# Optimization experiments

Hardware: AMD Instinct MI355X
Metric: run time of the kernel (lower is better)

Reference implementation:

```python
import jax, jax.numpy as jnp
import numpy as np

B, T, D = 2, 2048, 2048
H, KV, DH = 16, 8, 128
N, W, K = 1024, 256, 8


def rotate_half(x):
    x1, x2 = x[..., : DH // 2], x[..., DH // 2 :]
    return jnp.concatenate((-x2, x1), axis=-1)


def setup_inputs() -> dict:
    key = jax.random.key(0)
    ks = jax.random.split(key, 10)
    hidden_states = jax.random.normal(ks[0], (B, T, D), dtype=jnp.float32)
    cos = jax.random.uniform(ks[1], (B, T, DH), dtype=jnp.float32, minval=-1.0, maxval=1.0)
    sin = jax.random.uniform(ks[2], (B, T, DH), dtype=jnp.float32, minval=-1.0, maxval=1.0)
    mem = jax.random.normal(ks[3], (B, N, D), dtype=jnp.float32)
    Wq = jax.random.normal(ks[4], (D, D), dtype=jnp.float32) * 0.02
    Wk = jax.random.normal(ks[5], (KV * DH, D), dtype=jnp.float32) * 0.02
    Wv = jax.random.normal(ks[6], (KV * DH, D), dtype=jnp.float32) * 0.02
    Wo = jax.random.normal(ks[7], (D, D), dtype=jnp.float32) * 0.02
    Wg = jnp.zeros((1, D), dtype=jnp.float32)          # module inits gate weight to zeros
    bg = jnp.full((1,), 2.0, dtype=jnp.float32)        # and gate bias to 2.0
    return dict(hidden_states=hidden_states, cos=cos, sin=sin, mem=mem,
                Wq=Wq, Wk=Wk, Wv=Wv, Wo=Wo, Wg=Wg, bg=bg)


def reference(hidden_states, cos, sin, mem, Wq, Wk, Wv, Wo, Wg, bg):
    scale = DH ** -0.5
    n_rep = H // KV
    # projections -> [B, heads, T, d_h]
    q = (hidden_states @ Wq.T).reshape(B, T, H, DH).transpose(0, 2, 1, 3)
    k = (hidden_states @ Wk.T).reshape(B, T, KV, DH).transpose(0, 2, 1, 3)
    v = (hidden_states @ Wv.T).reshape(B, T, KV, DH).transpose(0, 2, 1, 3)
    # rotary (cos/sin are [B,T,d_h] -> broadcast over heads)
    c, s = cos[:, None], sin[:, None]
    q = q * c + rotate_half(q) * s
    k = k * c + rotate_half(k) * s
    # GQA repeat kv heads
    k_local = jnp.repeat(k, n_rep, axis=1)
    v_local = jnp.repeat(v, n_rep, axis=1)
    # --- local sliding-window causal attention (dense TxT mask, as in SDPA path) ---
    row = jnp.arange(T)[:, None]
    col = jnp.arange(T)[None, :]
    allowed = (col <= row) & (col >= row - W + 1)
    bias = jnp.where(allowed, 0.0, -jnp.inf).astype(q.dtype)
    scores = jnp.einsum('bhtd,bhsd->bhts', q, k_local) * scale + bias
    o_local = jnp.einsum('bhts,bhsd->bhtd', jax.nn.softmax(scores, axis=-1), v_local)
    o_local = o_local.transpose(0, 2, 1, 3).reshape(B, T, D) @ Wo.T
    # --- memory retrieval path (memory is detached in the original) ---
    mem_c = jax.lax.stop_gradient(mem)
    k_mem = (mem_c @ Wk.T).reshape(B, N, KV, DH).transpose(0, 2, 1, 3)
    v_mem = (mem_c @ Wv.T).reshape(B, N, KV, DH).transpose(0, 2, 1, 3)
    k_mem = jnp.repeat(k_mem, n_rep, axis=1)  # [B,H,N,d_h]
    v_mem = jnp.repeat(v_mem, n_rep, axis=1)
    q_chunk = q.mean(axis=2)                  # [B,H,d_h]
    sim_chunk = jnp.einsum('bhd,bhnd->bhn', q_chunk, k_mem) * scale
    _, idx = jax.lax.top_k(sim_chunk, K)      # [B,H,K]
    k_sh = jnp.take_along_axis(k_mem, idx[..., None], axis=2)  # [B,H,K,d_h]
    v_sh = jnp.take_along_axis(v_mem, idx[..., None], axis=2)
    sim_tok = jnp.einsum('bhtd,bhkd->bhtk', q, k_sh) * scale
    o_mem = jnp.einsum('bhtk,bhkd->bhtd', jax.nn.softmax(sim_tok, axis=-1), v_sh)
    o_mem = o_mem.transpose(0, 2, 1, 3).reshape(B, T, D)
    # --- learned gate fusion ---
    g = jax.nn.sigmoid(hidden_states @ Wg.T + bg)  # [B,T,1]
    return g * o_local + (1.0 - g) * o_mem
```

## Files before the change

### kernel.cpp

```cpp
#include <hip/hip_runtime.h>
#include <stdint.h>

#define B_   2
#define T_   2048
#define D_   2048
#define H_   16
#define KV_  8
#define DH_  128
#define NMEM 1024
#define WWIN 256
#define KSEL 8
#define BT   (B_*T_)
#define KVSTR 2048
#define QKVSTR 4096

__constant__ const float kScale = 0.08838834764831845f;

typedef __attribute__((ext_vector_type(8))) short s16x8;
typedef __attribute__((ext_vector_type(4))) float f32x4;

__device__ inline unsigned short f2bf(float f) {
  union { float f; unsigned int u; } c; c.f = f;
  unsigned int u = c.u;
  unsigned int r = u + 0x7fffu + ((u >> 16) & 1u);
  return (unsigned short)(r >> 16);
}
__device__ inline float bf2f(unsigned short v) {
  union { unsigned int u; float f; } c; c.u = ((unsigned int)v) << 16;
  return c.f;
}
__device__ inline f32x4 fzero4() { f32x4 v; v[0]=0.f; v[1]=0.f; v[2]=0.f; v[3]=0.f; return v; }

__global__ __launch_bounds__(256) void conv_kernel(const float* __restrict__ src,
                                                   unsigned short* __restrict__ dst, int n) {
  int i = blockIdx.x * 256 + threadIdx.x;
  if (i * 4 >= n) return;
  float4 v = ((const float4*)src)[i];
  uint2 o;
  o.x = (unsigned)f2bf(v.x) | ((unsigned)f2bf(v.y) << 16);
  o.y = (unsigned)f2bf(v.z) | ((unsigned)f2bf(v.w) << 16);
  ((uint2*)dst)[i] = o;
}

#define AOFF(buf, half) ((buf)*32768 + (half)*16384)
#define BOFF(buf, half) (65536 + (buf)*32768 + (half)*16384)

#define PH_MFMA(P, BF) \
  { \
    _Pragma("unroll") \
    for (int mi = 0; mi < 2; ++mi) { \
      _Pragma("unroll") \
      for (int ni = 0; ni < 4; ++ni) { \
        acc[P][mi][ni] = __builtin_amdgcn_mfma_f32_16x16x32_bf16(af[mi][0], BF[ni][0], acc[P][mi][ni], 0, 0, 0); \
        acc[P][mi][ni] = __builtin_amdgcn_mfma_f32_16x16x32_bf16(af[mi][1], BF[ni][1], acc[P][mi][ni], 0, 0, 0); \
      } \
    } \
  }

template<int MODE>
__global__ __launch_bounds__(512, 2) void gemm256(const unsigned short* __restrict__ A,
                                                  const unsigned short* __restrict__ Bw,
                                                  int N, int K, int lda, int ldc,
                                                  unsigned short* __restrict__ Cb,
                                                  const float* __restrict__ g,
                                                  const unsigned short* __restrict__ omem,
                                                  float* __restrict__ dout) {
  __shared__ __align__(16) char lds[131072];
  const int tid = threadIdx.x;
  const int wv = tid >> 6, lane = tid & 63;
  const int l15 = lane & 15, lg = lane >> 4;
  const int wr = wv >> 1, wc = wv & 1;
  const int gx = gridDim.x;
  const int nwg = gx * gridDim.y;
  const int flat = blockIdx.y * gx + blockIdx.x;
  const int chunk = nwg >> 3;
  const int wg = (flat & 7) * chunk + (flat >> 3);
  const int bx = wg % gx, by = wg / gx;
  const int m0 = by * 256, n0 = bx * 256;
  const int NT = K >> 6;

  auto stage_half = [&](const unsigned short* base, int stride, int row0, int koff, int ldsoff) {
#pragma unroll
    for (int ld = 0; ld < 2; ++ld) {
      int s = ld * 512 + tid;
      int row = s >> 3, cs = s & 7;
      int cg = cs ^ (row & 7);
      const unsigned short* src = base + (size_t)(row0 + row) * stride + koff + cg * 8;
      __builtin_amdgcn_global_load_lds((const __attribute__((address_space(1))) void*)src,
          (__attribute__((address_space(3))) void*)(lds + ldsoff + ld * 8192 + wv * 1024), 16, 0, 0);
    }
  };
  auto rdA = [&](int buf, int half, int mi, int kk) -> s16x8 {
    int r = wr * 32 + mi * 16 + l15;
    int slot = (kk * 4 + lg) ^ (r & 7);
    return *(const s16x8*)(lds + AOFF(buf, half) + r * 128 + slot * 16);
  };
  auto rdB = [&](int buf, int half, int ni, int kk) -> s16x8 {
    int r = wc * 64 + ni * 16 + l15;
    int slot = (kk * 4 + lg) ^ (r & 7);
    return *(const s16x8*)(lds + BOFF(buf, half) + r * 128 + slot * 16);
  };

  f32x4 acc[4][2][4];
#pragma unroll
  for (int p = 0; p < 4; ++p)
#pragma unroll
    for (int mi = 0; mi < 2; ++mi)
#pragma unroll
      for (int ni = 0; ni < 4; ++ni) acc[p][mi][ni] = fzero4();

  stage_half(A,  lda, m0,       0,  AOFF(0, 0));
  stage_half(Bw, K,   n0,       0,  BOFF(0, 0));
  stage_half(A,  lda, m0 + 128, 0,  AOFF(0, 1));
  stage_half(Bw, K,   n0 + 128, 0,  BOFF(0, 1));
  stage_half(A,  lda, m0,       64, AOFF(1, 0));
  stage_half(Bw, K,   n0,       64, BOFF(1, 0));
  stage_half(A,  lda, m0 + 128, 64, AOFF(1, 1));
  asm volatile("s_waitcnt vmcnt(6)" ::: "memory");
  __builtin_amdgcn_s_barrier();

  int cur = 0;
  for (int t = 0; t < NT; ++t, cur ^= 1) {
    const int nxt = cur ^ 1;
    s16x8 af[2][2], b0f[4][2], b1f[4][2];
#pragma unroll
    for (int mi = 0; mi < 2; ++mi) {
      af[mi][0] = rdA(cur, 0, mi, 0);
      af[mi][1] = rdA(cur, 0, mi, 1);
    }
#pragma unroll
    for (int ni = 0; ni < 4; ++ni) {
      b0f[ni][0] = rdB(cur, 0, ni, 0);
      b0f[ni][1] = rdB(cur, 0, ni, 1);
    }
    if (t + 1 < NT) stage_half(Bw, K, n0 + 128, (t + 1) * 64, BOFF(nxt, 1));
    __builtin_amdgcn_sched_barrier(0);
    __builtin_amdgcn_s_barrier();
    asm volatile("s_waitcnt lgkmcnt(0)" ::: "memory");
    __builtin_amdgcn_sched_barrier(0);
    __builtin_amdgcn_s_setprio(1);
    PH_MFMA(0, b0f);
    __builtin_amdgcn_s_setprio(0);
    __builtin_amdgcn_s_barrier();
#pragma unroll
    for (int ni = 0; ni < 4; ++ni) {
      b1f[ni][0] = rdB(cur, 1, ni, 0);
      b1f[ni][1] = rdB(cur, 1, ni, 1);
    }
    if (t + 2 < NT) stage_half(A, lda, m0, (t + 2) * 64, AOFF(cur, 0));
    __builtin_amdgcn_sched_barrier(0);
    __builtin_amdgcn_s_barrier();
    asm volatile("s_waitcnt lgkmcnt(0)" ::: "memory");
    __builtin_amdgcn_sched_barrier(0);
    __builtin_amdgcn_s_setprio(1);
    PH_MFMA(1, b1f);
    __builtin_amdgcn_s_setprio(0);
    __builtin_amdgcn_s_barrier();
#pragma unroll
    for (int mi = 0; mi < 2; ++mi) {
      af[mi][0] = rdA(cur, 1, mi, 0);
      af[mi][1] = rdA(cur, 1, mi, 1);
    }
    if (t + 2 < NT) stage_half(Bw, K, n0, (t + 2) * 64, BOFF(cur, 0));
    __builtin_amdgcn_sched_barrier(0);
    __builtin_amdgcn_s_barrier();
    asm volatile("s_waitcnt lgkmcnt(0)" ::: "memory");
    __builtin_amdgcn_sched_barrier(0);
    __builtin_amdgcn_s_setprio(1);
    PH_MFMA(2, b0f);
    __builtin_amdgcn_s_setprio(0);
    __builtin_amdgcn_s_barrier();
    if (t + 2 < NT) stage_half(A, lda, m0 + 128, (t + 2) * 64, AOFF(cur, 1));
    __builtin_amdgcn_sched_barrier(0);
    __builtin_amdgcn_s_barrier();
    __builtin_amdgcn_s_setprio(1);
    PH_MFMA(3, b1f);
    __builtin_amdgcn_s_setprio(0);
    if (t < NT - 2) asm volatile("s_waitcnt vmcnt(6)" ::: "memory");
    else            asm volatile("s_waitcnt vmcnt(0)" ::: "memory");
    __builtin_amdgcn_s_barrier();
  }

#pragma unroll
  for (int p = 0; p < 4; ++p)
#pragma unroll
    for (int mi = 0; mi < 2; ++mi)
#pragma unroll
      for (int ni = 0; ni < 4; ++ni)
#pragma unroll
        for (int j = 0; j < 4; ++j) {
          int row_g = m0 + (p >> 1) * 128 + wr * 32 + mi * 16 + lg * 4 + j;
          int col_g = n0 + (p & 1) * 128 + wc * 64 + ni * 16 + l15;
          float v = acc[p][mi][ni][j];
          size_t o = (size_t)row_g * ldc + col_g;
          if constexpr (MODE == 0) {
            Cb[o] = f2bf(v);
          } else {
            float gv = g[row_g];
            dout[o] = gv * v + (1.f - gv) * bf2f(omem[o]);
          }
        }
}

template<int MODE>
__global__ __launch_bounds__(256) void gemm_bt(const unsigned short* __restrict__ A,
                                               const unsigned short* __restrict__ Bw,
                                               int N, int K, int lda, int ldc,
                                               unsigned short* __restrict__ Cb,
                                               const float* __restrict__ g,
                                               const unsigned short* __restrict__ omem,
                                               float* __restrict__ dout) {
  __shared__ __align__(16) unsigned short sA[128 * 32];
  __shared__ __align__(16) unsigned short sB[128 * 32];
  const int tid = threadIdx.x;
  const int wv = tid >> 6, lane = tid & 63;
  const int gx = gridDim.x;
  const int nwg = gx * gridDim.y;
  const int flat = blockIdx.y * gx + blockIdx.x;
  const int chunk = nwg >> 3;
  const int wg = (flat & 7) * chunk + (flat >> 3);
  const int bx = wg % gx, by = wg / gx;
  const int m0 = by * 128, n0 = bx * 128;
  const int wr = wv >> 1, wc = wv & 1;
  const int l15 = lane & 15, lg = lane >> 4;
  const int rowA = tid >> 2;
  const int colB = (tid & 3) * 16;
  f32x4 acc[4][4];
#pragma unroll
  for (int mi = 0; mi < 4; ++mi)
#pragma unroll
    for (int ni = 0; ni < 4; ++ni) acc[mi][ni] = fzero4();

  char* sAc = (char*)sA;
  char* sBc = (char*)sB;
  for (int k0 = 0; k0 < K; k0 += 32) {
#pragma unroll
    for (int e = 0; e < 2; ++e) {
      const char* ga = (const char*)(A + ((size_t)(m0 + rowA + e * 64) * lda + k0)) + colB;
      __builtin_amdgcn_global_load_lds((const __attribute__((address_space(1))) void*)ga,
          (__attribute__((address_space(3))) void*)(sAc + e * 4096 + wv * 1024), 16, 0, 0);
      const char* gb = (const char*)(Bw + ((size_t)(n0 + rowA + e * 64) * K + k0)) + colB;
      __builtin_amdgcn_global_load_lds((const __attribute__((address_space(1))) void*)gb,
          (__attribute__((address_space(3))) void*)(sBc + e * 4096 + wv * 1024), 16, 0, 0);
    }
    __syncthreads();
    s16x8 af[4], bf_[4];
#pragma unroll
    for (int mi = 0; mi < 4; ++mi)
      af[mi] = *(const s16x8*)&sA[(wr * 64 + mi * 16 + l15) * 32 + lg * 8];
#pragma unroll
    for (int ni = 0; ni < 4; ++ni)
      bf_[ni] = *(const s16x8*)&sB[(wc * 64 + ni * 16 + l15) * 32 + lg * 8];
#pragma unroll
    for (int mi = 0; mi < 4; ++mi)
#pragma unroll
      for (int ni = 0; ni < 4; ++ni)
        acc[mi][ni] = __builtin_amdgcn_mfma_f32_16x16x32_bf16(af[mi], bf_[ni], acc[mi][ni], 0, 0, 0);
    __syncthreads();
  }
#pragma unroll
  for (int mi = 0; mi < 4; ++mi)
#pragma unroll
    for (int ni = 0; ni < 4; ++ni)
#pragma unroll
      for (int j = 0; j < 4; ++j) {
        int row_g = m0 + wr * 64 + mi * 16 + lg * 4 + j;
        int col_g = n0 + wc * 64 + ni * 16 + l15;
        float v = acc[mi][ni][j];
        size_t o = (size_t)row_g * ldc + col_g;
        if constexpr (MODE == 0) {
          Cb[o] = f2bf(v);
        } else {
          float gv = g[row_g];
          float om = bf2f(omem[o]);
          dout[o] = gv * v + (1.f - gv) * om;
        }
      }
}

__global__ __launch_bounds__(256) void rope_ip_kernel(unsigned short* __restrict__ buf,
                                                      const float* __restrict__ cosp,
                                                      const float* __restrict__ sinp,
                                                      int logp, int stride, int nthreads) {
  int i = blockIdx.x * 256 + threadIdx.x;
  if (i >= nthreads) return;
  int pp = i * 8;
  int row = pp >> logp;
  int p0 = pp & ((1 << logp) - 1);
  int blk = p0 >> 6, dd0 = p0 & 63;
  int b = row >> 11, t = row & 2047;
  const float* cb = cosp + ((size_t)b * T_ + t) * DH_;
  const float* sb = sinp + ((size_t)b * T_ + t) * DH_;
  unsigned short* p1 = buf + (size_t)row * stride + blk * 128 + dd0;
  s16x8 a = *(s16x8*)p1;
  s16x8 b8 = *(s16x8*)(p1 + 64);
  s16x8 o1, o2;
#pragma unroll
  for (int e = 0; e < 8; ++e) {
    float c1 = cb[dd0 + e], s1 = sb[dd0 + e];
    float c2 = cb[dd0 + 64 + e], s2 = sb[dd0 + 64 + e];
    float x1 = bf2f((unsigned short)a[e]), x2 = bf2f((unsigned short)b8[e]);
    o1[e] = (short)f2bf(x1 * c1 - x2 * s1);
    o2[e] = (short)f2bf(x2 * c2 + x1 * s2);
  }
  *(s16x8*)p1 = o1;
  *(s16x8*)(p1 + 64) = o2;
}

__global__ __launch_bounds__(256) void cs_kernel(const float* __restrict__ hs,
                                                 const float* __restrict__ cosp,
                                                 const float* __restrict__ sinp,
                                                 float* __restrict__ Cp, float* __restrict__ Sp) {
  __shared__ __align__(16) float hsL[32][128];
  __shared__ __align__(16) float csL[32][32];
  __shared__ __align__(16) float snL[32][32];
  const int tid = threadIdx.x;
  const int j0 = blockIdx.x * 128, d0 = blockIdx.y * 32;
  const int b = blockIdx.z >> 3, sp = blockIdx.z & 7;
  const int dq = (tid & 7) * 4;
  const int jq = (tid >> 3) * 4;
  float4 aC[4], aS[4];
#pragma unroll
  for (int a = 0; a < 4; ++a) {
    aC[a] = make_float4(0.f, 0.f, 0.f, 0.f);
    aS[a] = make_float4(0.f, 0.f, 0.f, 0.f);
  }
  const int csrow = tid >> 3, csc4 = tid & 7;
  for (int tile = 0; tile < 8; ++tile) {
    int t0 = sp * 256 + tile * 32;
    const float4* hs4 = (const float4*)(hs + ((size_t)b * T_ + t0) * D_ + j0);
#pragma unroll
    for (int r = 0; r < 4; ++r) {
      int i = tid + r * 256;
      int row = i >> 5, c4 = i & 31;
      *(float4*)&hsL[row][c4 * 4] = hs4[(size_t)row * (D_ / 4) + c4];
    }
    const float4* cp4 = (const float4*)(cosp + ((size_t)b * T_ + t0) * DH_ + d0);
    const float4* sp4 = (const float4*)(sinp + ((size_t)b * T_ + t0) * DH_ + d0);
    *(float4*)&csL[csrow][csc4 * 4] = cp4[(size_t)csrow * (DH_ / 4) + csc4];
    *(float4*)&snL[csrow][csc4 * 4] = sp4[(size_t)csrow * (DH_ / 4) + csc4];
    __syncthreads();
#pragma unroll 8
    for (int tt = 0; tt < 32; ++tt) {
      float4 cv = *(const float4*)&csL[tt][dq];
      float4 sv = *(const float4*)&snL[tt][dq];
      float4 hv = *(const float4*)&hsL[tt][jq];
      float ca[4] = {cv.x, cv.y, cv.z, cv.w};
      float sa[4] = {sv.x, sv.y, sv.z, sv.w};
#pragma unroll
      for (int a = 0; a < 4; ++a) {
        aC[a].x += ca[a] * hv.x; aC[a].y += ca[a] * hv.y;
        aC[a].z += ca[a] * hv.z; aC[a].w += ca[a] * hv.w;
        aS[a].x += sa[a] * hv.x; aS[a].y += sa[a] * hv.y;
        aS[a].z += sa[a] * hv.z; aS[a].w += sa[a] * hv.w;
      }
    }
    __syncthreads();
  }
#pragma unroll
  for (int a = 0; a < 4; ++a) {
    size_t o = ((size_t)(sp * B_ + b) * DH_ + d0 + dq + a) * D_ + j0 + jq;
    *(float4*)&Cp[o] = aC[a];
    *(float4*)&Sp[o] = aS[a];
  }
}

__global__ __launch_bounds__(256) void reduce_cs_kernel(const float4* __restrict__ Cp,
                                                        const float4* __restrict__ Sp,
                                                        float4* __restrict__ Cr,
                                                        float4* __restrict__ Sr) {
  int i = blockIdx.x * 256 + threadIdx.x;
  const int str = (B_ * DH_ * D_) / 4;
  float4 c = Cp[i], s = Sp[i];
#pragma unroll
  for (int p = 1; p < 8; ++p) {
    float4 cp = Cp[i + (size_t)p * str], sq = Sp[i + (size_t)p * str];
    c.x += cp.x; c.y += cp.y; c.z += cp.z; c.w += cp.w;
    s.x += sq.x; s.y += sq.y; s.z += sq.z; s.w += sq.w;
  }
  Cr[i] = c; Sr[i] = s;
}

__global__ __launch_bounds__(256) void qchunk_kernel(const float* __restrict__ Wq,
                                                     const float* __restrict__ Cr,
                                                     const float* __restrict__ Sr,
                                                     float* __restrict__ qc) {
  int gid = blockIdx.x * 256 + threadIdx.x;
  int wid = gid >> 6, lane = gid & 63;
  int b = wid >> 11, rem = wid & 2047;
  int h = rem >> 7, d = rem & 127;
  const float* w1 = Wq + (size_t)(h * DH_ + d) * D_;
  int dp = (d < 64) ? d + 64 : d - 64;
  float sgn = (d < 64) ? -1.f : 1.f;
  const float* w2 = Wq + (size_t)(h * DH_ + dp) * D_;
  const float* crow = Cr + ((size_t)b * DH_ + d) * D_;
  const float* srow = Sr + ((size_t)b * DH_ + d) * D_;
  float a1 = 0.f, a2 = 0.f;
  for (int j = lane; j < D_; j += 64) { a1 += w1[j] * crow[j]; a2 += w2[j] * srow[j]; }
#pragma unroll
  for (int off = 1; off < 64; off <<= 1) { a1 += __shfl_xor(a1, off); a2 += __shfl_xor(a2, off); }
  if (lane == 0) qc[wid] = (a1 + sgn * a2) * (1.f / (float)T_);
}

__global__ __launch_bounds__(256) void zk_kernel(const float* __restrict__ qc,
                                                 const float* __restrict__ Wk,
                                                 float* __restrict__ z) {
  int j = blockIdx.x * 256 + threadIdx.x;
  int h = blockIdx.y, b = blockIdx.z;
  int kvh = h >> 1;
  const float* qcl = qc + ((size_t)b * H_ + h) * DH_;
  const float* wb = Wk + (size_t)kvh * DH_ * D_ + j;
  float acc = 0.f;
#pragma unroll 8
  for (int d = 0; d < 128; ++d) acc += qcl[d] * wb[(size_t)d * D_];
  z[((size_t)b * H_ + h) * D_ + j] = acc;
}

__global__ __launch_bounds__(256) void sim_kernel(const float* __restrict__ z,
                                                  const float* __restrict__ mem,
                                                  float* __restrict__ sim) {
  __shared__ float4 mL[16 * 512];
  int tid = threadIdx.x;
  int n0 = blockIdx.x * 16, b = blockIdx.y;
  const float4* mem4 = (const float4*)(mem + (size_t)b * NMEM * D_);
#pragma unroll
  for (int c = 0; c < 32; ++c) {
    int i = tid + c * 256;
    int r = i >> 9, j4 = i & 511;
    mL[r * 512 + (j4 ^ (r & 7))] = mem4[(size_t)(n0 + r) * 512 + j4];
  }
  __syncthreads();
  int h = tid >> 4, n = tid & 15;
  const float4* zr = (const float4*)(z + ((size_t)b * H_ + h) * D_);
  float acc = 0.f;
  for (int j4 = 0; j4 < 512; ++j4) {
    float4 zz = zr[j4];
    float4 mm = mL[n * 512 + (j4 ^ (n & 7))];
    acc += zz.x * mm.x + zz.y * mm.y + zz.z * mm.z + zz.w * mm.w;
  }
  sim[((size_t)b * H_ + h) * NMEM + n0 + n] = acc * kScale;
}

__global__ __launch_bounds__(256) void topk_kernel(const float* __restrict__ sim,
                                                   int* __restrict__ idx) {
  __shared__ float sL[1024];
  __shared__ float rv[256];
  __shared__ int ri[256];
  int tid = threadIdx.x;
  int h = blockIdx.x, b = blockIdx.y;
  const float* sp = sim + ((size_t)b * H_ + h) * NMEM;
#pragma unroll
  for (int r = 0; r < 4; ++r) sL[tid + r * 256] = sp[tid + r * 256];
  __syncthreads();
  for (int kk = 0; kk < 8; ++kk) {
    float bv = -INFINITY; int bi = 0x7fffffff;
#pragma unroll
    for (int r = 0; r < 4; ++r) {
      int i = tid + r * 256;
      float v = sL[i];
      if (v > bv || (v == bv && i < bi)) { bv = v; bi = i; }
    }
    rv[tid] = bv; ri[tid] = bi;
    __syncthreads();
    for (int s = 128; s > 0; s >>= 1) {
      if (tid < s) {
        float v2 = rv[tid + s]; int i2 = ri[tid + s];
        if (v2 > rv[tid] || (v2 == rv[tid] && i2 < ri[tid])) { rv[tid] = v2; ri[tid] = i2; }
      }
      __syncthreads();
    }
    if (tid == 0) { idx[((size_t)b * H_ + h) * KSEL + kk] = ri[0]; sL[ri[0]] = -INFINITY; }
    __syncthreads();
  }
}

__global__ __launch_bounds__(256) void memattn_kernel(const unsigned short* __restrict__ qbf,
                                                      const unsigned short* __restrict__ kvmem,
                                                      const int* __restrict__ idx,
                                                      unsigned short* __restrict__ omem) {
  __shared__ float kl[8][128];
  __shared__ float vl[8][128];
  __shared__ int selL[8];
  int tid = threadIdx.x;
  int b = blockIdx.z, h = blockIdx.y, t = blockIdx.x * 256 + tid;
  int kvh = h >> 1;
  if (tid < 8) selL[tid] = idx[((size_t)b * H_ + h) * KSEL + tid];
  __syncthreads();
  {
    int r = tid >> 5, c4 = (tid & 31) * 4;
    size_t rb = ((size_t)b * NMEM + selL[r]) * (size_t)KVSTR;
    ushort4 k4 = *(const ushort4*)(kvmem + rb + kvh * DH_ + c4);
    ushort4 v4 = *(const ushort4*)(kvmem + rb + KV_ * DH_ + kvh * DH_ + c4);
    kl[r][c4 + 0] = bf2f(k4.x); kl[r][c4 + 1] = bf2f(k4.y);
    kl[r][c4 + 2] = bf2f(k4.z); kl[r][c4 + 3] = bf2f(k4.w);
    vl[r][c4 + 0] = bf2f(v4.x); vl[r][c4 + 1] = bf2f(v4.y);
    vl[r][c4 + 2] = bf2f(v4.z); vl[r][c4 + 3] = bf2f(v4.w);
  }
  __syncthreads();
  float sc[8] = {0.f,0.f,0.f,0.f,0.f,0.f,0.f,0.f};
  const unsigned short* qr = qbf + (size_t)(b * T_ + t) * QKVSTR + h * DH_;
  for (int c = 0; c < 4; ++c) {
    const s16x8* qp = (const s16x8*)(qr + c * 32);
#pragma unroll
    for (int u = 0; u < 4; ++u) {
      s16x8 q8 = qp[u];
#pragma unroll
      for (int e = 0; e < 8; ++e) {
        float qv = bf2f((unsigned short)q8[e]);
        int d = c * 32 + u * 8 + e;
#pragma unroll
        for (int kk = 0; kk < 8; ++kk) sc[kk] += qv * kl[kk][d];
      }
    }
  }
  float sm[8], mx = -INFINITY;
#pragma unroll
  for (int kk = 0; kk < 8; ++kk) { sm[kk] = sc[kk] * kScale; mx = fmaxf(mx, sm[kk]); }
  float sum = 0.f;
#pragma unroll
  for (int kk = 0; kk < 8; ++kk) { sm[kk] = __expf(sm[kk] - mx); sum += sm[kk]; }
  float inv = 1.f / sum;
#pragma unroll
  for (int kk = 0; kk < 8; ++kk) sm[kk] *= inv;
  unsigned short* orow = omem + (size_t)(b * T_ + t) * D_ + h * DH_;
  for (int d = 0; d < 128; d += 4) {
    float o0 = 0.f, o1 = 0.f, o2 = 0.f, o3 = 0.f;
#pragma unroll
    for (int kk = 0; kk < 8; ++kk) {
      float w = sm[kk];
      o0 += w * vl[kk][d + 0];
      o1 += w * vl[kk][d + 1];
      o2 += w * vl[kk][d + 2];
      o3 += w * vl[kk][d + 3];
    }
    uint2 pk;
    pk.x = (unsigned)f2bf(o0) | ((unsigned)f2bf(o1) << 16);
    pk.y = (unsigned)f2bf(o2) | ((unsigned)f2bf(o3) << 16);
    *(uint2*)(orow + d) = pk;
  }
}

__global__ __launch_bounds__(256) void gate_kernel(const float* __restrict__ hs,
                                                   const float* __restrict__ Wg,
                                                   const float* __restrict__ bg,
                                                   float* __restrict__ g) {
  int gid = blockIdx.x * 256 + threadIdx.x;
  int row = gid >> 6, lane = gid & 63;
  const float4* hr = (const float4*)(hs + (size_t)row * D_);
  const float4* wg4 = (const float4*)Wg;
  float acc = 0.f;
#pragma unroll
  for (int it = 0; it < 8; ++it) {
    float4 hv = hr[lane + it * 64], wv = wg4[lane + it * 64];
    acc += hv.x * wv.x + hv.y * wv.y + hv.z * wv.z + hv.w * wv.w;
  }
#pragma unroll
  for (int off = 1; off < 64; off <<= 1) acc += __shfl_xor(acc, off);
  if (lane == 0) g[row] = 1.f / (1.f + __expf(-(acc + bg[0])));
}

__global__ __launch_bounds__(256) void localattn_kernel(const unsigned short* __restrict__ qbf,
                                                        const unsigned short* __restrict__ kbf,
                                                        const unsigned short* __restrict__ vbf,
                                                        unsigned short* __restrict__ olocal) {
  __shared__ __align__(16) unsigned short pl[4][16][40];
  const int tid = threadIdx.x;
  const int w = tid >> 6, lane = tid & 63;
  const int tb = blockIdx.x * 64;
  const int h = blockIdx.y, b = blockIdx.z;
  const int kvh = h >> 1;
  const int t0 = tb + w * 16;
  const int l15 = lane & 15, lg = lane >> 4;

  s16x8 qf[4];
  {
    const unsigned short* qb = qbf + ((size_t)(b * T_ + t0 + l15) * QKVSTR) + h * DH_ + lg * 8;
#pragma unroll
    for (int kb = 0; kb < 4; ++kb) qf[kb] = *(const s16x8*)(qb + kb * 32);
  }
  f32x4 of[8];
#pragma unroll
  for (int nb = 0; nb < 8; ++nb) of[nb] = fzero4();
  float m_r[4] = {-INFINITY, -INFINITY, -INFINITY, -INFINITY};
  float l_r[4] = {0.f, 0.f, 0.f, 0.f};

  int sstart = t0 - (WWIN - 1);
  if (sstart < 0) sstart = 0;
  sstart &= ~31;
  for (int s0 = sstart; s0 <= t0 + 15; s0 += 32) {
    f32x4 sc[2];
    sc[0] = fzero4(); sc[1] = fzero4();
    const unsigned short* kb0 = kbf + ((size_t)(b * T_ + s0 + l15) * QKVSTR) + kvh * DH_ + lg * 8;
#pragma unroll
    for (int cb = 0; cb < 2; ++cb) {
#pragma unroll
      for (int kb = 0; kb < 4; ++kb) {
        s16x8 kf = *(const s16x8*)(kb0 + (size_t)cb * 16 * QKVSTR + kb * 32);
        sc[cb] = __builtin_amdgcn_mfma_f32_16x16x32_bf16(qf[kb], kf, sc[cb], 0, 0, 0);
      }
    }
    float pv[2][4];
#pragma unroll
    for (int j = 0; j < 4; ++j) {
      int t = t0 + lg * 4 + j;
      int s_a = s0 + l15, s_b = s_a + 16;
      float va = sc[0][j] * kScale;
      float vb = sc[1][j] * kScale;
      va = (s_a <= t && s_a + (WWIN - 1) >= t) ? va : -INFINITY;
      vb = (s_b <= t && s_b + (WWIN - 1) >= t) ? vb : -INFINITY;
      float mx = fmaxf(va, vb);
#pragma unroll
      for (int off = 1; off < 16; off <<= 1) mx = fmaxf(mx, __shfl_xor(mx, off));
      float mn = fmaxf(m_r[j], mx);
      float alpha, pa, pb;
      if (mn == -INFINITY) { alpha = 1.f; pa = 0.f; pb = 0.f; }
      else {
        alpha = __expf(m_r[j] - mn);
        pa = __expf(va - mn);
        pb = __expf(vb - mn);
      }
      m_r[j] = mn;
      float rs = pa + pb;
#pragma unroll
      for (int off = 1; off < 16; off <<= 1) rs += __shfl_xor(rs, off);
      l_r[j] = l_r[j] * alpha + rs;
#pragma unroll
      for (int nb = 0; nb < 8; ++nb) of[nb][j] *= alpha;
      pv[0][j] = pa; pv[1][j] = pb;
    }
#pragma unroll
    for (int cb = 0; cb < 2; ++cb)
#pragma unroll
      for (int j = 0; j < 4; ++j)
        pl[w][lg * 4 + j][cb * 16 + l15] = f2bf(pv[cb][j]);
    asm volatile("s_waitcnt lgkmcnt(0)" ::: "memory");
    __builtin_amdgcn_sched_barrier(0);
    s16x8 pa8 = *(const s16x8*)&pl[w][l15][lg * 8];
    const unsigned short* vb0 = vbf + ((size_t)(b * T_ + s0 + lg * 8) * QKVSTR) + kvh * DH_ + l15;
#pragma unroll
    for (int nb = 0; nb < 8; ++nb) {
      s16x8 vf;
#pragma unroll
      for (int jj = 0; jj < 8; ++jj) vf[jj] = (short)vb0[(size_t)jj * QKVSTR + nb * 16];
      of[nb] = __builtin_amdgcn_mfma_f32_16x16x32_bf16(pa8, vf, of[nb], 0, 0, 0);
    }
  }
  float inv[4];
#pragma unroll
  for (int j = 0; j < 4; ++j) inv[j] = 1.f / l_r[j];
#pragma unroll
  for (int nb = 0; nb < 8; ++nb)
#pragma unroll
    for (int j = 0; j < 4; ++j) {
      int t = t0 + lg * 4 + j;
      olocal[(size_t)(b * T_ + t) * QKVSTR + h * DH_ + nb * 16 + l15] = f2bf(of[nb][j] * inv[j]);
    }
}

extern "C" void kernel_launch(void* const* d_in, const int* in_sizes, int n_in,
                              void* d_out, int out_size, void* d_ws, size_t ws_size,
                              hipStream_t stream) {
  const float* hs   = (const float*)d_in[0];
  const float* cosp = (const float*)d_in[1];
  const float* sinp = (const float*)d_in[2];
  const float* mem  = (const float*)d_in[3];
  const float* Wq   = (const float*)d_in[4];
  const float* Wk   = (const float*)d_in[5];
  const float* Wv   = (const float*)d_in[6];
  const float* Wo   = (const float*)d_in[7];
  const float* Wg   = (const float*)d_in[8];
  const float* bg   = (const float*)d_in[9];
  float* out = (float*)d_out;

  char* p = (char*)d_ws;
  auto alloc = [&](size_t bytes) { char* r = p; p += (bytes + 255) & ~(size_t)255; return r; };
  float* qc     = (float*)alloc((size_t)B_ * H_ * DH_ * 4);
  float* gbuf   = (float*)alloc((size_t)BT * 4);
  float* zbuf   = (float*)alloc((size_t)B_ * H_ * D_ * 4);
  float* simbuf = (float*)alloc((size_t)B_ * H_ * NMEM * 4);
  int*   idxbuf = (int*)alloc((size_t)B_ * H_ * KSEL * 4);
  unsigned short* hs_bf   = (unsigned short*)alloc((size_t)BT * D_ * 2);
  unsigned short* qkv_raw = (unsigned short*)alloc((size_t)BT * QKVSTR * 2);
  unsigned short* wbig    = (unsigned short*)alloc((size_t)2 * D_ * D_ * 2);
  unsigned short* mem_bf  = (unsigned short*)alloc((size_t)B_ * NMEM * D_ * 2);
  unsigned short* kvmem   = (unsigned short*)alloc((size_t)B_ * NMEM * KVSTR * 2);

  float* Cp = (float*)d_out;
  float* Sp = Cp + (size_t)8 * B_ * DH_ * D_;
  float* Cr = (float*)mem_bf;
  float* Sr = Cr + (size_t)B_ * DH_ * D_;
  unsigned short* omem_bf = hs_bf;

  conv_kernel<<<(BT * D_ / 4 + 255) / 256, 256, 0, stream>>>(hs, hs_bf, BT * D_);
  conv_kernel<<<(D_ * D_ / 4 + 255) / 256, 256, 0, stream>>>(Wq, wbig, D_ * D_);
  conv_kernel<<<(KV_ * DH_ * D_ / 4 + 255) / 256, 256, 0, stream>>>(Wk, wbig + (size_t)D_ * D_, KV_ * DH_ * D_);
  conv_kernel<<<(KV_ * DH_ * D_ / 4 + 255) / 256, 256, 0, stream>>>(Wv, wbig + (size_t)D_ * D_ + (size_t)KV_ * DH_ * D_, KV_ * DH_ * D_);
  gemm256<0><<<dim3(QKVSTR / 256, BT / 256), 512, 0, stream>>>(hs_bf, wbig, QKVSTR, D_, D_, QKVSTR, qkv_raw, nullptr, nullptr, nullptr);
  conv_kernel<<<(B_ * NMEM * D_ / 4 + 255) / 256, 256, 0, stream>>>(mem, mem_bf, B_ * NMEM * D_);
  gemm_bt<0><<<dim3(KVSTR / 128, (B_ * NMEM) / 128), 256, 0, stream>>>(mem_bf, wbig + (size_t)D_ * D_, KVSTR, D_, D_, KVSTR, kvmem, nullptr, nullptr, nullptr);

  rope_ip_kernel<<<(BT * D_ / 16 + 255) / 256, 256, 0, stream>>>(qkv_raw, cosp, sinp, 10, QKVSTR, BT * D_ / 16);
  rope_ip_kernel<<<(BT * KV_ * DH_ / 16 + 255) / 256, 256, 0, stream>>>(qkv_raw + D_, cosp, sinp, 9, QKVSTR, BT * KV_ * DH_ / 16);

  cs_kernel<<<dim3(D_ / 128, DH_ / 32, B_ * 8), 256, 0, stream>>>(hs, cosp, sinp, Cp, Sp);
  reduce_cs_kernel<<<(B_ * DH_ * D_ / 4) / 256, 256, 0, stream>>>((const float4*)Cp, (const float4*)Sp, (float4*)Cr, (float4*)Sr);
  qchunk_kernel<<<(B_ * H_ * DH_) / 4, 256, 0, stream>>>(Wq, Cr, Sr, qc);
  zk_kernel<<<dim3(D_ / 256, H_, B_), 256, 0, stream>>>(qc, Wk, zbuf);
  sim_kernel<<<dim3(NMEM / 16, B_), 256, 0, stream>>>(zbuf, mem, simbuf);
  topk_kernel<<<dim3(H_, B_), 256, 0, stream>>>(simbuf, idxbuf);

  memattn_kernel<<<dim3(T_ / 256, H_, B_), 256, 0, stream>>>(qkv_raw, kvmem, idxbuf, omem_bf);

  gate_kernel<<<BT / 4, 256, 0, stream>>>(hs, Wg, bg, gbuf);

  localattn_kernel<<<dim3(T_ / 64, H_, B_), 256, 0, stream>>>(qkv_raw, qkv_raw + D_, qkv_raw + D_ + KV_ * DH_, qkv_raw);

  conv_kernel<<<(D_ * D_ / 4 + 255) / 256, 256, 0, stream>>>(Wo, wbig, D_ * D_);
  gemm256<1><<<dim3(D_ / 256, BT / 256), 512, 0, stream>>>(qkv_raw, wbig, D_, D_, QKVSTR, D_, nullptr, gbuf, omem_bf, out);
}
```

Baseline: 462.8 us.

## Stage K/V tiles in LDS with double buffering for local attention

The local attention kernel now stages each 32-row K tile and a transposed V tile in LDS, shared across the block's four waves. K uses global_load_lds with an XOR swizzle, V is transposed into LDS with a swizzle, and the next tile is prefetched into the other buffer while the current one is consumed. This replaces per-wave global K loads and the very strided scalar 2-byte V gathers. The price is that every wave now iterates over the block-wide key range, including some fully masked chunks, plus a __syncthreads per iteration and more LDS use that may lower occupancy.

```diff
diff --git a/kernel.cpp b/kernel.cpp
--- a/kernel.cpp
+++ b/kernel.cpp
@@ -563,6 +563,8 @@
                                                         const unsigned short* __restrict__ kbf,
                                                         const unsigned short* __restrict__ vbf,
                                                         unsigned short* __restrict__ olocal) {
+  __shared__ __align__(16) unsigned short kL[2][32][128];
+  __shared__ __align__(16) unsigned short vL[2][128][32];
   __shared__ __align__(16) unsigned short pl[4][16][40];
   const int tid = threadIdx.x;
   const int w = tid >> 6, lane = tid & 63;
@@ -584,18 +586,50 @@
   float m_r[4] = {-INFINITY, -INFINITY, -INFINITY, -INFINITY};
   float l_r[4] = {0.f, 0.f, 0.f, 0.f};
 
-  int sstart = t0 - (WWIN - 1);
+  int sstart = tb - (WWIN - 1);
   if (sstart < 0) sstart = 0;
   sstart &= ~31;
-  for (int s0 = sstart; s0 <= t0 + 15; s0 += 32) {
+  const int slast = tb + 63;
+
+  auto STAGE = [&](int buf, int s0) {
+#pragma unroll
+    for (int ld = 0; ld < 2; ++ld) {
+      int s = ld * 256 + tid;
+      int r = s >> 4, cs = s & 15;
+      int cg = cs ^ (r & 7);
+      const unsigned short* src = kbf + (size_t)(b * T_ + s0 + r) * QKVSTR + kvh * DH_ + cg * 8;
+      __builtin_amdgcn_global_load_lds((const __attribute__((address_space(1))) void*)src,
+          (__attribute__((address_space(3))) void*)((char*)&kL[buf][0][0] + ld * 4096 + w * 1024), 16, 0, 0);
+    }
+#pragma unroll
+    for (int it = 0; it < 2; ++it) {
+      int idx = it * 256 + tid;
+      int r = idx >> 4, c0 = (idx & 15) * 8;
+      s16x8 v8 = *(const s16x8*)(vbf + (size_t)(b * T_ + s0 + r) * QKVSTR + kvh * DH_ + c0);
+      int q = r >> 3, e0 = r & 7;
+#pragma unroll
+      for (int e = 0; e < 8; ++e) {
+        int c = c0 + e;
+        vL[buf][c][(q ^ (c & 3)) * 8 + e0] = (unsigned short)v8[e];
+      }
+    }
+  };
+
+  STAGE(0, sstart);
+  int buf = 0;
+  for (int s0 = sstart; s0 <= slast; s0 += 32, buf ^= 1) {
+    __syncthreads();
+    if (s0 + 32 <= slast) STAGE(buf ^ 1, s0 + 32);
+
     f32x4 sc[2];
     sc[0] = fzero4(); sc[1] = fzero4();
-    const unsigned short* kb0 = kbf + ((size_t)(b * T_ + s0 + l15) * QKVSTR) + kvh * DH_ + lg * 8;
 #pragma unroll
     for (int cb = 0; cb < 2; ++cb) {
 #pragma unroll
       for (int kb = 0; kb < 4; ++kb) {
-        s16x8 kf = *(const s16x8*)(kb0 + (size_t)cb * 16 * QKVSTR + kb * 32);
+        int r = cb * 16 + l15;
+        int c = kb * 4 + lg;
+        s16x8 kf = *(const s16x8*)((char*)&kL[buf][0][0] + r * 256 + ((c ^ (r & 7)) * 16));
         sc[cb] = __builtin_amdgcn_mfma_f32_16x16x32_bf16(qf[kb], kf, sc[cb], 0, 0, 0);
       }
     }
@@ -636,15 +670,14 @@
     asm volatile("s_waitcnt lgkmcnt(0)" ::: "memory");
     __builtin_amdgcn_sched_barrier(0);
     s16x8 pa8 = *(const s16x8*)&pl[w][l15][lg * 8];
-    const unsigned short* vb0 = vbf + ((size_t)(b * T_ + s0 + lg * 8) * QKVSTR) + kvh * DH_ + l15;
 #pragma unroll
     for (int nb = 0; nb < 8; ++nb) {
-      s16x8 vf;
-#pragma unroll
-      for (int jj = 0; jj < 8; ++jj) vf[jj] = (short)vb0[(size_t)jj * QKVSTR + nb * 16];
+      int c = nb * 16 + l15;
+      s16x8 vf = *(const s16x8*)&vL[buf][c][(lg ^ (c & 3)) * 8];
       of[nb] = __builtin_amdgcn_mfma_f32_16x16x32_bf16(pa8, vf, of[nb], 0, 0, 0);
     }
   }
+
   float inv[4];
 #pragma unroll
   for (int j = 0; j < 4; ++j) inv[j] = 1.f / l_r[j];
```

Result: no change. 461.6 us (-0.3%).
